# Performance work log

Hardware: AMD Instinct MI355X
Metric: run time of the kernel (lower is better)

The kernel has to match this reference:

```python
import jax, jax.numpy as jnp
import numpy as np

VOCAB, EMB, HID = 32000, 512, 1024

def setup_inputs() -> dict:
    key = jax.random.key(0)
    k1, k2, k3, k4, k5, k6 = jax.random.split(key, 6)
    s_e = 1.0 / np.sqrt(EMB)
    s_h = 1.0 / np.sqrt(HID)
    return {
        "x": jax.random.randint(k1, (32, 512), 0, VOCAB, dtype=jnp.int64),
        "emb_table": jax.random.normal(k2, (VOCAB, EMB), dtype=jnp.float32),
        "W_ih": jax.random.uniform(k3, (4 * HID, EMB), jnp.float32, -s_h, s_h),
        "W_hh": jax.random.uniform(k4, (4 * HID, HID), jnp.float32, -s_h, s_h),
        "b_ih": jax.random.uniform(k5, (4 * HID,), jnp.float32, -s_h, s_h),
        "b_hh": jax.random.uniform(k6, (4 * HID,), jnp.float32, -s_h, s_h),
    }

def _lstm(embedded, W_ih, W_hh, b_ih, b_hh):
    # embedded: [B, T, E]; gates order (PyTorch): i, f, g, o
    B = embedded.shape[0]
    H = W_hh.shape[1]
    # Precompute input projections for all timesteps: [B, T, 4H]
    x_proj = jnp.einsum('bte,ge->btg', embedded, W_ih) + b_ih + b_hh

    def step(carry, xt):
        h, c = carry
        gates = xt + h @ W_hh.T  # [B, 4H]
        i, f, g, o = jnp.split(gates, 4, axis=-1)
        i = jax.nn.sigmoid(i)
        f = jax.nn.sigmoid(f)
        g = jnp.tanh(g)
        o = jax.nn.sigmoid(o)
        c = f * c + i * g
        h = o * jnp.tanh(c)
        return (h, c), h

    h0 = jnp.zeros((B, H), embedded.dtype)
    c0 = jnp.zeros((B, H), embedded.dtype)
    (h_f, c_f), hs = jax.lax.scan(step, (h0, c0), jnp.swapaxes(x_proj, 0, 1))
    return jnp.swapaxes(hs, 0, 1), h_f, c_f

def reference(x, emb_table, W_ih, W_hh, b_ih, b_hh):
    embedded = emb_table[x]  # [B, T, E]
    encoder_outputs, state_h, state_c = _lstm(embedded, W_ih, W_hh, b_ih, b_hh)
    return encoder_outputs, state_h, state_c
```

## Files before the change

kernel.cpp:

```cpp
#include <hip/hip_runtime.h>

#define Bb 32
#define Tt 512
#define Ee 512
#define Hh 1024
#define NSLOT 256

typedef __attribute__((ext_vector_type(8))) short bf16x8;
typedef __attribute__((ext_vector_type(4))) float f32x4;
typedef unsigned long long u64;

__device__ __forceinline__ unsigned short f2bf(float f) {
  unsigned int u = __float_as_uint(f);
  u = (u + 0x7fffu + ((u >> 16) & 1u)) >> 16;
  return (unsigned short)u;
}
__device__ __forceinline__ float bf2f(unsigned short s) {
  return __uint_as_float(((unsigned int)s) << 16);
}
__device__ __forceinline__ float sigmoidf_(float x) {
  x = fminf(fmaxf(x, -30.f), 30.f);
  return 1.f / (1.f + __expf(-x));
}
__device__ __forceinline__ float tanh_fast(float x) {
  float xx = fminf(fmaxf(x, -15.f), 15.f);
  float e = __expf(2.f * xx);
  return (e - 1.f) / (e + 1.f);
}

__global__ void gather_kernel(const int* __restrict__ x,
                              const float* __restrict__ emb,
                              unsigned short* __restrict__ emb_hi,
                              unsigned short* __restrict__ emb_lo,
                              unsigned short* __restrict__ hbuf,
                              unsigned* __restrict__ bar) {
  long long gid = (long long)blockIdx.x * blockDim.x + threadIdx.x;
  long long stride = (long long)gridDim.x * blockDim.x;
  for (long long i = gid; i < 8192; i += stride)
    ((ushort4*)hbuf)[i] = make_ushort4(0, 0, 0, 0);
  for (long long i = gid; i < 1024; i += stride)
    bar[i] = 0u;
  long long n4 = (long long)Bb * Tt * Ee / 4;
  for (long long i = gid; i < n4; i += stride) {
    long long bt = i >> 7;
    int e4 = (int)(i & 127);
    int row = x[bt];
    row = min(max(row, 0), 31999);
    float4 v = ((const float4*)(emb + (long long)row * Ee))[e4];
    ushort4 hv, lv;
    hv.x = f2bf(v.x); lv.x = f2bf(v.x - bf2f(hv.x));
    hv.y = f2bf(v.y); lv.y = f2bf(v.y - bf2f(hv.y));
    hv.z = f2bf(v.z); lv.z = f2bf(v.z - bf2f(hv.z));
    hv.w = f2bf(v.w); lv.w = f2bf(v.w - bf2f(hv.w));
    ((ushort4*)emb_hi)[i] = hv;
    ((ushort4*)emb_lo)[i] = lv;
  }
}

__global__ __launch_bounds__(256, 1)
void lstm_kernel(const unsigned short* __restrict__ emb_hi,
                 const unsigned short* __restrict__ emb_lo,
                 unsigned short* __restrict__ hbuf,
                 unsigned* __restrict__ bar,
                 const float* __restrict__ W_ih,
                 const float* __restrict__ W_hh,
                 const float* __restrict__ b_ih,
                 const float* __restrict__ b_hh,
                 float* __restrict__ out) {
  __shared__ unsigned short sWih_hi[16 * 512];
  __shared__ unsigned short sWih_lo[16 * 512];
  __shared__ unsigned short sWhh_hi[16 * 1024];
  __shared__ unsigned short sWhh_lo[16 * 1024];
  __shared__ float sAcc[2][4][2][16][17];
  __shared__ float sBias[16];
  __shared__ float sC[32][4];

  const int tid = threadIdx.x;
  const int lane = tid & 63;
  const int wv = tid >> 6;
  const int wg = blockIdx.x;
  const int j0 = (wg & 7) * 128 + (wg >> 3) * 4;
  const int gflag = (wg & 7) * 4 + (wg >> 6);

  for (int idx = tid; idx < 16 * 64; idx += 256) {
    int c = idx >> 6, kc8 = idx & 63;
    int grow = (c >> 2) * Hh + j0 + (c & 3);
    const float* src = W_ih + (long long)grow * Ee + kc8 * 8;
    int us = (c * 512 + kc8 * 8) ^ ((c & 7) << 3);
#pragma unroll
    for (int j = 0; j < 8; j++) {
      float f = src[j];
      unsigned short h = f2bf(f);
      sWih_hi[us + j] = h;
      sWih_lo[us + j] = f2bf(f - bf2f(h));
    }
  }
  for (int idx = tid; idx < 16 * 128; idx += 256) {
    int c = idx >> 7, kc8 = idx & 127;
    int grow = (c >> 2) * Hh + j0 + (c & 3);
    const float* src = W_hh + (long long)grow * Hh + kc8 * 8;
    int us = (c * 1024 + kc8 * 8) ^ ((c & 7) << 3);
#pragma unroll
    for (int j = 0; j < 8; j++) {
      float f = src[j];
      unsigned short h = f2bf(f);
      sWhh_hi[us + j] = h;
      sWhh_lo[us + j] = f2bf(f - bf2f(h));
    }
  }
  if (tid < 16) {
    int grow = (tid >> 2) * Hh + j0 + (tid & 3);
    sBias[tid] = b_ih[grow] + b_hh[grow];
  }
  if (tid < 128) sC[tid >> 2][tid & 3] = 0.f;
  __syncthreads();

  const int r16 = lane & 15;
  const int kg = (lane >> 4) * 8;
  const int col = lane & 15;
  const int xr = (col & 7) << 3;

  const unsigned* fp = bar + (unsigned)(wv + 4 * (lane & 7)) * 16;

  float h_last = 0.f, c_last = 0.f;

  for (int t = 0; t < Tt; t++) {
    f32x4 acc[2][3];
#pragma unroll
    for (int mt = 0; mt < 2; mt++)
#pragma unroll
      for (int cb = 0; cb < 3; cb++)
        acc[mt][cb] = (f32x4){0.f, 0.f, 0.f, 0.f};

#pragma unroll
    for (int q = 0; q < 4; q++) {
      int kc = wv + q * 4;
      int bo = (col * 512 + kc * 32 + kg) ^ xr;
      bf16x8 bH = *(const bf16x8*)(sWih_hi + bo);
      bf16x8 bL = *(const bf16x8*)(sWih_lo + bo);
#pragma unroll
      for (int mt = 0; mt < 2; mt++) {
        int rb = mt * 16 + r16;
        int ai = (rb * Tt + t) * Ee + kc * 32 + kg;
        bf16x8 aH = *(const bf16x8*)(emb_hi + ai);
        bf16x8 aL = *(const bf16x8*)(emb_lo + ai);
        acc[mt][0] = __builtin_amdgcn_mfma_f32_16x16x32_bf16(aH, bH, acc[mt][0], 0, 0, 0);
        acc[mt][1] = __builtin_amdgcn_mfma_f32_16x16x32_bf16(aH, bL, acc[mt][1], 0, 0, 0);
        acc[mt][2] = __builtin_amdgcn_mfma_f32_16x16x32_bf16(aL, bH, acc[mt][2], 0, 0, 0);
      }
    }

    {
      unsigned target = 16u * (unsigned)t;
      while (__any(__hip_atomic_load(fp, __ATOMIC_RELAXED,
                                     __HIP_MEMORY_SCOPE_AGENT) < target))
        __builtin_amdgcn_s_sleep(1);
    }
    __builtin_amdgcn_sched_barrier(0);

    const unsigned short* hb = hbuf + (unsigned)(t & (NSLOT - 1)) * 32768;
#pragma unroll
    for (int q = 0; q < 8; q++) {
      int kc = wv + q * 4;
      int bo = (col * 1024 + kc * 32 + kg) ^ xr;
      bf16x8 bH = *(const bf16x8*)(sWhh_hi + bo);
      bf16x8 bL = *(const bf16x8*)(sWhh_lo + bo);
#pragma unroll
      for (int mt = 0; mt < 2; mt++) {
        int rb = mt * 16 + r16;
        bf16x8 aH = *(const bf16x8*)(hb + rb * Hh + kc * 32 + kg);
        acc[mt][0] = __builtin_amdgcn_mfma_f32_16x16x32_bf16(aH, bH, acc[mt][0], 0, 0, 0);
        acc[mt][1] = __builtin_amdgcn_mfma_f32_16x16x32_bf16(aH, bL, acc[mt][1], 0, 0, 0);
      }
    }

#pragma unroll
    for (int mt = 0; mt < 2; mt++) {
      f32x4 tot = acc[mt][0] + acc[mt][1] + acc[mt][2];
#pragma unroll
      for (int r = 0; r < 4; r++)
        sAcc[t & 1][wv][mt][(lane >> 4) * 4 + r][col] = tot[r];
    }
    __syncthreads();

    if (tid < 128) {
      int b = tid >> 2, du = tid & 3;
      int mt = b >> 4, rr = b & 15;
      float g0 = sBias[0 * 4 + du], g1 = sBias[1 * 4 + du];
      float g2 = sBias[2 * 4 + du], g3 = sBias[3 * 4 + du];
#pragma unroll
      for (int w = 0; w < 4; w++) {
        g0 += sAcc[t & 1][w][mt][rr][0 * 4 + du];
        g1 += sAcc[t & 1][w][mt][rr][1 * 4 + du];
        g2 += sAcc[t & 1][w][mt][rr][2 * 4 + du];
        g3 += sAcc[t & 1][w][mt][rr][3 * 4 + du];
      }
      float ig = sigmoidf_(g0);
      float fg = sigmoidf_(g1);
      float gg = tanh_fast(g2);
      float og = sigmoidf_(g3);
      float cn = fg * sC[b][du] + ig * gg;
      sC[b][du] = cn;
      float hn = og * tanh_fast(cn);
      h_last = hn; c_last = cn;

      unsigned pack = (unsigned)f2bf(hn);
      unsigned other = __shfl_xor(pack, 1, 64);
      unsigned* nb32 =
          (unsigned*)(hbuf + (unsigned)((t + 1) & (NSLOT - 1)) * 32768);
      if ((du & 1) == 0) {
        unsigned w = (pack & 0xffffu) | (other << 16);
        __hip_atomic_store(nb32 + ((b * 1024 + j0 + du) >> 1), w,
                           __ATOMIC_RELAXED, __HIP_MEMORY_SCOPE_AGENT);
      }
      asm volatile("s_waitcnt vmcnt(0)" ::: "memory");
      if ((tid & 63) == 0)
        __hip_atomic_fetch_add(bar + gflag * 16, 1u, __ATOMIC_RELAXED,
                               __HIP_MEMORY_SCOPE_AGENT);
      out[((long long)b * Tt + t) * Hh + j0 + du] = hn;
    }
  }

  if (tid < 128) {
    int b = tid >> 2, du = tid & 3;
    int hj = j0 + du;
    out[16777216LL + b * Hh + hj] = h_last;
    out[16777216LL + 32768 + b * Hh + hj] = c_last;
  }
}

extern "C" void kernel_launch(void* const* d_in, const int* in_sizes, int n_in,
                              void* d_out, int out_size, void* d_ws, size_t ws_size,
                              hipStream_t stream) {
  const int* x      = (const int*)d_in[0];
  const float* emb  = (const float*)d_in[1];
  const float* W_ih = (const float*)d_in[2];
  const float* W_hh = (const float*)d_in[3];
  const float* b_ih = (const float*)d_in[4];
  const float* b_hh = (const float*)d_in[5];
  float* out = (float*)d_out;

  unsigned short* emb_hi = (unsigned short*)d_ws;
  unsigned short* emb_lo = emb_hi + 8388608;
  unsigned short* hbuf   = emb_lo + 8388608;
  unsigned*       bar    = (unsigned*)(hbuf + 8388608);

  hipLaunchKernelGGL(gather_kernel, dim3(2048), dim3(256), 0, stream,
                     x, emb, emb_hi, emb_lo, hbuf, bar);

  void* args[] = { (void*)&emb_hi, (void*)&emb_lo, (void*)&hbuf, (void*)&bar,
                   (void*)&W_ih, (void*)&W_hh, (void*)&b_ih, (void*)&b_hh,
                   (void*)&out };
  hipLaunchCooperativeKernel((void*)lstm_kernel, dim3(256), dim3(256), args, 0, stream);
}
```

Before: 3.464 ms.

## Restructure grid barrier: one poller wave, intra-block drain handshake, fewer global flags

Changes the cross-workgroup step barrier. Each group of four workgroups now shares one flag counter, 64 flags in total. Only wave 0 polls the flags, with a short spin before it starts sleeping, and a __syncthreads releases the other waves. Inside each block, wave 1 signals through a shared-memory variable once its stores have drained, so only one thread per block does a global atomic add. The aim is less atomic traffic and polling contention on the global flags, at the cost of an extra block-wide barrier on the critical path every step.

```diff
diff --git a/kernel.cpp b/kernel.cpp
--- a/kernel.cpp
+++ b/kernel.cpp
@@ -74,13 +74,14 @@
   __shared__ float sAcc[2][4][2][16][17];
   __shared__ float sBias[16];
   __shared__ float sC[32][4];
+  __shared__ unsigned sDrain;
 
   const int tid = threadIdx.x;
   const int lane = tid & 63;
   const int wv = tid >> 6;
   const int wg = blockIdx.x;
   const int j0 = (wg & 7) * 128 + (wg >> 3) * 4;
-  const int gflag = (wg & 7) * 4 + (wg >> 6);
+  const int fg = wg >> 2;
 
   for (int idx = tid; idx < 16 * 64; idx += 256) {
     int c = idx >> 6, kc8 = idx & 63;
@@ -113,14 +114,13 @@
     sBias[tid] = b_ih[grow] + b_hh[grow];
   }
   if (tid < 128) sC[tid >> 2][tid & 3] = 0.f;
+  if (tid == 0) sDrain = 0u;
   __syncthreads();
 
   const int r16 = lane & 15;
   const int kg = (lane >> 4) * 8;
   const int col = lane & 15;
   const int xr = (col & 7) << 3;
-
-  const unsigned* fp = bar + (unsigned)(wv + 4 * (lane & 7)) * 16;
 
   float h_last = 0.f, c_last = 0.f;
 
@@ -150,12 +150,18 @@
       }
     }
 
-    {
-      unsigned target = 16u * (unsigned)t;
-      while (__any(__hip_atomic_load(fp, __ATOMIC_RELAXED,
-                                     __HIP_MEMORY_SCOPE_AGENT) < target))
-        __builtin_amdgcn_s_sleep(1);
-    }
+    if (wv == 0) {
+      const unsigned* fpl = bar + (unsigned)lane * 16;
+      unsigned tgt = 4u * (unsigned)t;
+      int it = 0;
+      for (;;) {
+        unsigned v = __hip_atomic_load(fpl, __ATOMIC_RELAXED,
+                                       __HIP_MEMORY_SCOPE_AGENT);
+        if (!__any(v < tgt)) break;
+        if (++it > 2) __builtin_amdgcn_s_sleep(8);
+      }
+    }
+    __syncthreads();
     __builtin_amdgcn_sched_barrier(0);
 
     const unsigned short* hb = hbuf + (unsigned)(t & (NSLOT - 1)) * 32768;
@@ -196,10 +202,10 @@
         g3 += sAcc[t & 1][w][mt][rr][3 * 4 + du];
       }
       float ig = sigmoidf_(g0);
-      float fg = sigmoidf_(g1);
+      float fg2 = sigmoidf_(g1);
       float gg = tanh_fast(g2);
       float og = sigmoidf_(g3);
-      float cn = fg * sC[b][du] + ig * gg;
+      float cn = fg2 * sC[b][du] + ig * gg;
       sC[b][du] = cn;
       float hn = og * tanh_fast(cn);
       h_last = hn; c_last = cn;
@@ -214,9 +220,15 @@
                            __ATOMIC_RELAXED, __HIP_MEMORY_SCOPE_AGENT);
       }
       asm volatile("s_waitcnt vmcnt(0)" ::: "memory");
-      if ((tid & 63) == 0)
-        __hip_atomic_fetch_add(bar + gflag * 16, 1u, __ATOMIC_RELAXED,
+      if (tid == 64)
+        __hip_atomic_store(&sDrain, (unsigned)(t + 1), __ATOMIC_RELEASE,
+                           __HIP_MEMORY_SCOPE_WORKGROUP);
+      if (tid == 0) {
+        while (__hip_atomic_load(&sDrain, __ATOMIC_ACQUIRE,
+                                 __HIP_MEMORY_SCOPE_WORKGROUP) < (unsigned)(t + 1)) {}
+        __hip_atomic_fetch_add(bar + fg * 16, 1u, __ATOMIC_RELAXED,
                                __HIP_MEMORY_SCOPE_AGENT);
+      }
       out[((long long)b * Tt + t) * Hh + j0 + du] = hn;
     }
   }
```

Result: slower. 3.710 ms (+7.1%).

## Collapse LSTM block to a single wavefront with shuffle-based gate gather

Applied to the files above, without the earlier changes.

Each workgroup shrinks from four wavefronts to one. That one wave does the whole K reduction for its 16 gate columns, so the LDS partial-sum exchange and the __syncthreads per timestep go away. Gates are regrouped with cross-lane shuffles, and the cell state stays in registers. The input projection for the next step is computed after publishing h, so it sits off the critical path between barrier waits. The trade-off is four times more serial MFMA work per wave on the recurrent path, with less latency hiding.

```diff
diff --git a/kernel.cpp b/kernel.cpp
--- a/kernel.cpp
+++ b/kernel.cpp
@@ -57,7 +57,7 @@
   }
 }
 
-__global__ __launch_bounds__(256, 1)
+__global__ __launch_bounds__(64, 1)
 void lstm_kernel(const unsigned short* __restrict__ emb_hi,
                  const unsigned short* __restrict__ emb_lo,
                  unsigned short* __restrict__ hbuf,
@@ -71,18 +71,15 @@
   __shared__ unsigned short sWih_lo[16 * 512];
   __shared__ unsigned short sWhh_hi[16 * 1024];
   __shared__ unsigned short sWhh_lo[16 * 1024];
-  __shared__ float sAcc[2][4][2][16][17];
-  __shared__ float sBias[16];
-  __shared__ float sC[32][4];
+  __shared__ unsigned short sHpub[32][4];
+  __shared__ float sHout[32][4];
 
   const int tid = threadIdx.x;
-  const int lane = tid & 63;
-  const int wv = tid >> 6;
   const int wg = blockIdx.x;
   const int j0 = (wg & 7) * 128 + (wg >> 3) * 4;
   const int gflag = (wg & 7) * 4 + (wg >> 6);
 
-  for (int idx = tid; idx < 16 * 64; idx += 256) {
+  for (int idx = tid; idx < 16 * 64; idx += 64) {
     int c = idx >> 6, kc8 = idx & 63;
     int grow = (c >> 2) * Hh + j0 + (c & 3);
     const float* src = W_ih + (long long)grow * Ee + kc8 * 8;
@@ -95,7 +92,7 @@
       sWih_lo[us + j] = f2bf(f - bf2f(h));
     }
   }
-  for (int idx = tid; idx < 16 * 128; idx += 256) {
+  for (int idx = tid; idx < 16 * 128; idx += 64) {
     int c = idx >> 7, kc8 = idx & 127;
     int grow = (c >> 2) * Hh + j0 + (c & 3);
     const float* src = W_hh + (long long)grow * Hh + kc8 * 8;
@@ -108,124 +105,140 @@
       sWhh_lo[us + j] = f2bf(f - bf2f(h));
     }
   }
-  if (tid < 16) {
-    int grow = (tid >> 2) * Hh + j0 + (tid & 3);
-    sBias[tid] = b_ih[grow] + b_hh[grow];
-  }
-  if (tid < 128) sC[tid >> 2][tid & 3] = 0.f;
-  __syncthreads();
-
-  const int r16 = lane & 15;
-  const int kg = (lane >> 4) * 8;
-  const int col = lane & 15;
-  const int xr = (col & 7) << 3;
-
-  const unsigned* fp = bar + (unsigned)(wv + 4 * (lane & 7)) * 16;
-
-  float h_last = 0.f, c_last = 0.f;
+
+  const int b0 = tid & 15;
+  const int du = tid >> 4;
+  const int kg = (tid >> 4) * 8;
+  const int cW = tid & 15;
+  const int xr = (cW & 7) << 3;
+
+  float bias_g[4];
+#pragma unroll
+  for (int g = 0; g < 4; g++)
+    bias_g[g] = b_ih[g * Hh + j0 + du] + b_hh[g * Hh + j0 + du];
+
+  float c_reg[2] = {0.f, 0.f};
+  float hL[2] = {0.f, 0.f}, cL[2] = {0.f, 0.f};
+
+  f32x4 xacc[2][3];
+  auto xproj = [&](int t) {
+#pragma unroll
+    for (int mt = 0; mt < 2; mt++)
+#pragma unroll
+      for (int cb = 0; cb < 3; cb++)
+        xacc[mt][cb] = (f32x4){0.f, 0.f, 0.f, 0.f};
+#pragma unroll
+    for (int q = 0; q < 16; q++) {
+      int bo = (cW * 512 + q * 32 + kg) ^ xr;
+      bf16x8 wH = *(const bf16x8*)(sWih_hi + bo);
+      bf16x8 wL = *(const bf16x8*)(sWih_lo + bo);
+#pragma unroll
+      for (int mt = 0; mt < 2; mt++) {
+        long long ai = ((long long)(mt * 16 + b0) * Tt + t) * Ee + q * 32 + kg;
+        bf16x8 eH = *(const bf16x8*)(emb_hi + ai);
+        bf16x8 eL = *(const bf16x8*)(emb_lo + ai);
+        xacc[mt][0] = __builtin_amdgcn_mfma_f32_16x16x32_bf16(wH, eH, xacc[mt][0], 0, 0, 0);
+        xacc[mt][1] = __builtin_amdgcn_mfma_f32_16x16x32_bf16(wL, eH, xacc[mt][1], 0, 0, 0);
+        xacc[mt][2] = __builtin_amdgcn_mfma_f32_16x16x32_bf16(wH, eL, xacc[mt][2], 0, 0, 0);
+      }
+    }
+  };
+  xproj(0);
 
   for (int t = 0; t < Tt; t++) {
-    f32x4 acc[2][3];
-#pragma unroll
-    for (int mt = 0; mt < 2; mt++)
-#pragma unroll
-      for (int cb = 0; cb < 3; cb++)
-        acc[mt][cb] = (f32x4){0.f, 0.f, 0.f, 0.f};
-
-#pragma unroll
-    for (int q = 0; q < 4; q++) {
-      int kc = wv + q * 4;
-      int bo = (col * 512 + kc * 32 + kg) ^ xr;
-      bf16x8 bH = *(const bf16x8*)(sWih_hi + bo);
-      bf16x8 bL = *(const bf16x8*)(sWih_lo + bo);
+    {
+      unsigned tgt = 8u * (unsigned)t;
+      for (;;) {
+        unsigned v = tgt;
+        if (tid < 32)
+          v = __hip_atomic_load(bar + (unsigned)tid * 16, __ATOMIC_RELAXED,
+                                __HIP_MEMORY_SCOPE_AGENT);
+        if (!__any(v < tgt)) break;
+        __builtin_amdgcn_s_sleep(1);
+      }
+    }
+    __builtin_amdgcn_sched_barrier(0);
+
+    const unsigned short* hb = hbuf + (unsigned)(t & (NSLOT - 1)) * 32768;
+    f32x4 racc[2][2];
+#pragma unroll
+    for (int mt = 0; mt < 2; mt++) {
+      racc[mt][0] = xacc[mt][0] + xacc[mt][2];
+      racc[mt][1] = xacc[mt][1];
+    }
+#pragma unroll
+    for (int q = 0; q < 32; q++) {
+      int bo = (cW * 1024 + q * 32 + kg) ^ xr;
+      bf16x8 wH = *(const bf16x8*)(sWhh_hi + bo);
+      bf16x8 wL = *(const bf16x8*)(sWhh_lo + bo);
 #pragma unroll
       for (int mt = 0; mt < 2; mt++) {
-        int rb = mt * 16 + r16;
-        int ai = (rb * Tt + t) * Ee + kc * 32 + kg;
-        bf16x8 aH = *(const bf16x8*)(emb_hi + ai);
-        bf16x8 aL = *(const bf16x8*)(emb_lo + ai);
-        acc[mt][0] = __builtin_amdgcn_mfma_f32_16x16x32_bf16(aH, bH, acc[mt][0], 0, 0, 0);
-        acc[mt][1] = __builtin_amdgcn_mfma_f32_16x16x32_bf16(aH, bL, acc[mt][1], 0, 0, 0);
-        acc[mt][2] = __builtin_amdgcn_mfma_f32_16x16x32_bf16(aL, bH, acc[mt][2], 0, 0, 0);
+        bf16x8 hf = *(const bf16x8*)(hb + (b0 + 16 * mt) * 1024 + q * 32 + kg);
+        racc[mt][0] = __builtin_amdgcn_mfma_f32_16x16x32_bf16(wH, hf, racc[mt][0], 0, 0, 0);
+        racc[mt][1] = __builtin_amdgcn_mfma_f32_16x16x32_bf16(wL, hf, racc[mt][1], 0, 0, 0);
       }
     }
 
-    {
-      unsigned target = 16u * (unsigned)t;
-      while (__any(__hip_atomic_load(fp, __ATOMIC_RELAXED,
-                                     __HIP_MEMORY_SCOPE_AGENT) < target))
-        __builtin_amdgcn_s_sleep(1);
-    }
-    __builtin_amdgcn_sched_barrier(0);
-
-    const unsigned short* hb = hbuf + (unsigned)(t & (NSLOT - 1)) * 32768;
-#pragma unroll
-    for (int q = 0; q < 8; q++) {
-      int kc = wv + q * 4;
-      int bo = (col * 1024 + kc * 32 + kg) ^ xr;
-      bf16x8 bH = *(const bf16x8*)(sWhh_hi + bo);
-      bf16x8 bL = *(const bf16x8*)(sWhh_lo + bo);
-#pragma unroll
-      for (int mt = 0; mt < 2; mt++) {
-        int rb = mt * 16 + r16;
-        bf16x8 aH = *(const bf16x8*)(hb + rb * Hh + kc * 32 + kg);
-        acc[mt][0] = __builtin_amdgcn_mfma_f32_16x16x32_bf16(aH, bH, acc[mt][0], 0, 0, 0);
-        acc[mt][1] = __builtin_amdgcn_mfma_f32_16x16x32_bf16(aH, bL, acc[mt][1], 0, 0, 0);
-      }
-    }
-
 #pragma unroll
     for (int mt = 0; mt < 2; mt++) {
-      f32x4 tot = acc[mt][0] + acc[mt][1] + acc[mt][2];
-#pragma unroll
-      for (int r = 0; r < 4; r++)
-        sAcc[t & 1][wv][mt][(lane >> 4) * 4 + r][col] = tot[r];
-    }
-    __syncthreads();
-
-    if (tid < 128) {
-      int b = tid >> 2, du = tid & 3;
-      int mt = b >> 4, rr = b & 15;
-      float g0 = sBias[0 * 4 + du], g1 = sBias[1 * 4 + du];
-      float g2 = sBias[2 * 4 + du], g3 = sBias[3 * 4 + du];
-#pragma unroll
-      for (int w = 0; w < 4; w++) {
-        g0 += sAcc[t & 1][w][mt][rr][0 * 4 + du];
-        g1 += sAcc[t & 1][w][mt][rr][1 * 4 + du];
-        g2 += sAcc[t & 1][w][mt][rr][2 * 4 + du];
-        g3 += sAcc[t & 1][w][mt][rr][3 * 4 + du];
-      }
-      float ig = sigmoidf_(g0);
-      float fg = sigmoidf_(g1);
-      float gg = tanh_fast(g2);
-      float og = sigmoidf_(g3);
-      float cn = fg * sC[b][du] + ig * gg;
-      sC[b][du] = cn;
-      float hn = og * tanh_fast(cn);
-      h_last = hn; c_last = cn;
-
-      unsigned pack = (unsigned)f2bf(hn);
-      unsigned other = __shfl_xor(pack, 1, 64);
-      unsigned* nb32 =
-          (unsigned*)(hbuf + (unsigned)((t + 1) & (NSLOT - 1)) * 32768);
-      if ((du & 1) == 0) {
-        unsigned w = (pack & 0xffffu) | (other << 16);
-        __hip_atomic_store(nb32 + ((b * 1024 + j0 + du) >> 1), w,
-                           __ATOMIC_RELAXED, __HIP_MEMORY_SCOPE_AGENT);
-      }
-      asm volatile("s_waitcnt vmcnt(0)" ::: "memory");
-      if ((tid & 63) == 0)
-        __hip_atomic_fetch_add(bar + gflag * 16, 1u, __ATOMIC_RELAXED,
-                               __HIP_MEMORY_SCOPE_AGENT);
-      out[((long long)b * Tt + t) * Hh + j0 + du] = hn;
-    }
-  }
-
-  if (tid < 128) {
-    int b = tid >> 2, du = tid & 3;
-    int hj = j0 + du;
-    out[16777216LL + b * Hh + hj] = h_last;
-    out[16777216LL + 32768 + b * Hh + hj] = c_last;
+      f32x4 v = racc[mt][0] + racc[mt][1];
+      float r0 = v[0], r1 = v[1], r2 = v[2], r3 = v[3];
+      float p0 = __shfl_xor(r0, 32), p1 = __shfl_xor(r1, 32);
+      float p2 = __shfl_xor(r2, 32), p3 = __shfl_xor(r3, 32);
+      bool lowg = (tid & 32) == 0;
+      float n0 = lowg ? r0 : p2, n1 = lowg ? r1 : p3;
+      float n2 = lowg ? p0 : r2, n3 = lowg ? p1 : r3;
+      float q0 = __shfl_xor(n0, 16), q1 = __shfl_xor(n1, 16);
+      float q2 = __shfl_xor(n2, 16), q3 = __shfl_xor(n3, 16);
+      bool eg = (tid & 16) == 0;
+      float gi = eg ? n0 : q1;
+      float gf = eg ? q0 : n1;
+      float gg = eg ? n2 : q3;
+      float go = eg ? q2 : n3;
+      float i_ = sigmoidf_(gi + bias_g[0]);
+      float f_ = sigmoidf_(gf + bias_g[1]);
+      float g_ = tanh_fast(gg + bias_g[2]);
+      float o_ = sigmoidf_(go + bias_g[3]);
+      float cn = f_ * c_reg[mt] + i_ * g_;
+      c_reg[mt] = cn;
+      float hn = o_ * tanh_fast(cn);
+      hL[mt] = hn; cL[mt] = cn;
+      int bg = b0 + 16 * mt;
+      sHpub[bg][du] = f2bf(hn);
+      sHout[bg][du] = hn;
+    }
+
+    if (tid < 32) {
+      u64 w = *(const u64*)&sHpub[tid][0];
+      u64* dst = (u64*)(hbuf + (unsigned)((t + 1) & (NSLOT - 1)) * 32768 +
+                        tid * 1024 + j0);
+      __hip_atomic_store(dst, w, __ATOMIC_RELAXED, __HIP_MEMORY_SCOPE_AGENT);
+    }
+    asm volatile("s_waitcnt vmcnt(0)" ::: "memory");
+    if (tid == 0)
+      __hip_atomic_fetch_add(bar + gflag * 16, 1u, __ATOMIC_RELAXED,
+                             __HIP_MEMORY_SCOPE_AGENT);
+
+    if (tid < 32) {
+      float4 vv = *(const float4*)&sHout[tid][0];
+      *(float4*)(out + ((long long)tid * Tt + t) * Hh + j0) = vv;
+    }
+
+    if (t + 1 < Tt) xproj(t + 1);
+  }
+
+  sHout[b0][du] = hL[0];
+  sHout[b0 + 16][du] = hL[1];
+  if (tid < 32) {
+    float4 vv = *(const float4*)&sHout[tid][0];
+    *(float4*)(out + 16777216LL + (long long)tid * Hh + j0) = vv;
+  }
+  __builtin_amdgcn_sched_barrier(0);
+  sHout[b0][du] = cL[0];
+  sHout[b0 + 16][du] = cL[1];
+  if (tid < 32) {
+    float4 vv = *(const float4*)&sHout[tid][0];
+    *(float4*)(out + 16777216LL + 32768 + (long long)tid * Hh + j0) = vv;
   }
 }
 
@@ -251,5 +264,5 @@
   void* args[] = { (void*)&emb_hi, (void*)&emb_lo, (void*)&hbuf, (void*)&bar,
                    (void*)&W_ih, (void*)&W_hh, (void*)&b_ih, (void*)&b_hh,
                    (void*)&out };
-  hipLaunchCooperativeKernel((void*)lstm_kernel, dim3(256), dim3(256), args, 0, stream);
-}
+  hipLaunchCooperativeKernel((void*)lstm_kernel, dim3(256), dim3(64), args, 0, stream);
+}
```

Result: slower. 10.15 ms (+193.0%).

## Replace counter barrier with sentinel-flagged hidden-state polling per timestep

Applied to the files above, without the earlier changes.

Drops the per-step atomic counter barrier. Each timestep's h buffer is now pre-filled with a NaN sentinel, and consumers poll the h data itself with atomic 64-bit loads until no sentinel remains. Producers pack four bf16 h values into one 64-bit atomic store, and the buffer grows to one slot per timestep (no ring reuse). This removes the fetch_add, the vmcnt wait and the flag spin, in exchange for a larger sentinel init in the gather kernel and a risk that a real bf16 value equal to the sentinel causes a hang.

```diff
diff --git a/kernel.cpp b/kernel.cpp
--- a/kernel.cpp
+++ b/kernel.cpp
@@ -4,11 +4,12 @@
 #define Tt 512
 #define Ee 512
 #define Hh 1024
-#define NSLOT 256
 
 typedef __attribute__((ext_vector_type(8))) short bf16x8;
 typedef __attribute__((ext_vector_type(4))) float f32x4;
 typedef unsigned long long u64;
+
+#define SEN 0x7FC0u
 
 __device__ __forceinline__ unsigned short f2bf(float f) {
   unsigned int u = __float_as_uint(f);
@@ -32,14 +33,15 @@
                               const float* __restrict__ emb,
                               unsigned short* __restrict__ emb_hi,
                               unsigned short* __restrict__ emb_lo,
-                              unsigned short* __restrict__ hbuf,
-                              unsigned* __restrict__ bar) {
+                              unsigned short* __restrict__ hbuf) {
   long long gid = (long long)blockIdx.x * blockDim.x + threadIdx.x;
   long long stride = (long long)gridDim.x * blockDim.x;
   for (long long i = gid; i < 8192; i += stride)
     ((ushort4*)hbuf)[i] = make_ushort4(0, 0, 0, 0);
-  for (long long i = gid; i < 1024; i += stride)
-    bar[i] = 0u;
+  for (long long i = 8192 + gid; i < 4194304; i += stride)
+    ((ushort4*)hbuf)[i] =
+        make_ushort4((unsigned short)SEN, (unsigned short)SEN,
+                     (unsigned short)SEN, (unsigned short)SEN);
   long long n4 = (long long)Bb * Tt * Ee / 4;
   for (long long i = gid; i < n4; i += stride) {
     long long bt = i >> 7;
@@ -61,7 +63,6 @@
 void lstm_kernel(const unsigned short* __restrict__ emb_hi,
                  const unsigned short* __restrict__ emb_lo,
                  unsigned short* __restrict__ hbuf,
-                 unsigned* __restrict__ bar,
                  const float* __restrict__ W_ih,
                  const float* __restrict__ W_hh,
                  const float* __restrict__ b_ih,
@@ -80,7 +81,6 @@
   const int wv = tid >> 6;
   const int wg = blockIdx.x;
   const int j0 = (wg & 7) * 128 + (wg >> 3) * 4;
-  const int gflag = (wg & 7) * 4 + (wg >> 6);
 
   for (int idx = tid; idx < 16 * 64; idx += 256) {
     int c = idx >> 6, kc8 = idx & 63;
@@ -117,10 +117,9 @@
 
   const int r16 = lane & 15;
   const int kg = (lane >> 4) * 8;
+  const int kgq = (lane >> 4) * 2;
   const int col = lane & 15;
   const int xr = (col & 7) << 3;
-
-  const unsigned* fp = bar + (unsigned)(wv + 4 * (lane & 7)) * 16;
 
   float h_last = 0.f, c_last = 0.f;
 
@@ -150,28 +149,34 @@
       }
     }
 
-    {
-      unsigned target = 16u * (unsigned)t;
-      while (__any(__hip_atomic_load(fp, __ATOMIC_RELAXED,
-                                     __HIP_MEMORY_SCOPE_AGENT) < target))
-        __builtin_amdgcn_s_sleep(1);
-    }
-    __builtin_amdgcn_sched_barrier(0);
-
-    const unsigned short* hb = hbuf + (unsigned)(t & (NSLOT - 1)) * 32768;
+    const u64* hb64 = (const u64*)hbuf + (u64)t * 8192;
 #pragma unroll
     for (int q = 0; q < 8; q++) {
       int kc = wv + q * 4;
+      int i0 = r16 * 256 + kc * 8 + kgq;
+      int i1 = (16 + r16) * 256 + kc * 8 + kgq;
+      u64 a0, a1, c0, c1;
+      for (;;) {
+        a0 = __hip_atomic_load(hb64 + i0, __ATOMIC_RELAXED, __HIP_MEMORY_SCOPE_AGENT);
+        a1 = __hip_atomic_load(hb64 + i0 + 1, __ATOMIC_RELAXED, __HIP_MEMORY_SCOPE_AGENT);
+        c0 = __hip_atomic_load(hb64 + i1, __ATOMIC_RELAXED, __HIP_MEMORY_SCOPE_AGENT);
+        c1 = __hip_atomic_load(hb64 + i1 + 1, __ATOMIC_RELAXED, __HIP_MEMORY_SCOPE_AGENT);
+        bool bad = ((unsigned)(a0 & 0xFFFFu) == SEN) |
+                   ((unsigned)(a1 & 0xFFFFu) == SEN) |
+                   ((unsigned)(c0 & 0xFFFFu) == SEN) |
+                   ((unsigned)(c1 & 0xFFFFu) == SEN);
+        if (!__any(bad)) break;
+      }
+      union { u64 q2[2]; bf16x8 v; } ua, uc;
+      ua.q2[0] = a0; ua.q2[1] = a1;
+      uc.q2[0] = c0; uc.q2[1] = c1;
       int bo = (col * 1024 + kc * 32 + kg) ^ xr;
       bf16x8 bH = *(const bf16x8*)(sWhh_hi + bo);
       bf16x8 bL = *(const bf16x8*)(sWhh_lo + bo);
-#pragma unroll
-      for (int mt = 0; mt < 2; mt++) {
-        int rb = mt * 16 + r16;
-        bf16x8 aH = *(const bf16x8*)(hb + rb * Hh + kc * 32 + kg);
-        acc[mt][0] = __builtin_amdgcn_mfma_f32_16x16x32_bf16(aH, bH, acc[mt][0], 0, 0, 0);
-        acc[mt][1] = __builtin_amdgcn_mfma_f32_16x16x32_bf16(aH, bL, acc[mt][1], 0, 0, 0);
-      }
+      acc[0][0] = __builtin_amdgcn_mfma_f32_16x16x32_bf16(ua.v, bH, acc[0][0], 0, 0, 0);
+      acc[0][1] = __builtin_amdgcn_mfma_f32_16x16x32_bf16(ua.v, bL, acc[0][1], 0, 0, 0);
+      acc[1][0] = __builtin_amdgcn_mfma_f32_16x16x32_bf16(uc.v, bH, acc[1][0], 0, 0, 0);
+      acc[1][1] = __builtin_amdgcn_mfma_f32_16x16x32_bf16(uc.v, bL, acc[1][1], 0, 0, 0);
     }
 
 #pragma unroll
@@ -204,19 +209,16 @@
       float hn = og * tanh_fast(cn);
       h_last = hn; c_last = cn;
 
-      unsigned pack = (unsigned)f2bf(hn);
-      unsigned other = __shfl_xor(pack, 1, 64);
-      unsigned* nb32 =
-          (unsigned*)(hbuf + (unsigned)((t + 1) & (NSLOT - 1)) * 32768);
-      if ((du & 1) == 0) {
-        unsigned w = (pack & 0xffffu) | (other << 16);
-        __hip_atomic_store(nb32 + ((b * 1024 + j0 + du) >> 1), w,
-                           __ATOMIC_RELAXED, __HIP_MEMORY_SCOPE_AGENT);
-      }
-      asm volatile("s_waitcnt vmcnt(0)" ::: "memory");
-      if ((tid & 63) == 0)
-        __hip_atomic_fetch_add(bar + gflag * 16, 1u, __ATOMIC_RELAXED,
-                               __HIP_MEMORY_SCOPE_AGENT);
+      unsigned p16 = (unsigned)f2bf(hn);
+      unsigned o1 = __shfl_xor(p16, 1, 64);
+      unsigned v32 = ((du & 1) == 0) ? ((p16 & 0xffffu) | (o1 << 16))
+                                     : (((o1 & 0xffffu)) | (p16 << 16));
+      unsigned o2 = __shfl_xor(v32, 2, 64);
+      if (t + 1 < Tt && du == 0) {
+        u64 w = (u64)v32 | ((u64)o2 << 32);
+        u64* dst = (u64*)hbuf + (u64)(t + 1) * 8192 + b * 256 + (j0 >> 2);
+        __hip_atomic_store(dst, w, __ATOMIC_RELAXED, __HIP_MEMORY_SCOPE_AGENT);
+      }
       out[((long long)b * Tt + t) * Hh + j0 + du] = hn;
     }
   }
@@ -243,12 +245,11 @@
   unsigned short* emb_hi = (unsigned short*)d_ws;
   unsigned short* emb_lo = emb_hi + 8388608;
   unsigned short* hbuf   = emb_lo + 8388608;
-  unsigned*       bar    = (unsigned*)(hbuf + 8388608);
 
   hipLaunchKernelGGL(gather_kernel, dim3(2048), dim3(256), 0, stream,
-                     x, emb, emb_hi, emb_lo, hbuf, bar);
-
-  void* args[] = { (void*)&emb_hi, (void*)&emb_lo, (void*)&hbuf, (void*)&bar,
+                     x, emb, emb_hi, emb_lo, hbuf);
+
+  void* args[] = { (void*)&emb_hi, (void*)&emb_lo, (void*)&hbuf,
                    (void*)&W_ih, (void*)&W_hh, (void*)&b_ih, (void*)&b_hh,
                    (void*)&out };
   hipLaunchCooperativeKernel((void*)lstm_kernel, dim3(256), dim3(256), args, 0, stream);
```

Result: slower. 3.853 ms (+11.2%).
